# Optimization experiments

Measured on AMD Instinct MI355X. Metric: run time of the kernel, lower is better.

Reference implementation:

```python
import jax, jax.numpy as jnp
import numpy as np

K = 5  # kernel_size, n_qubits = K*K = 25
PAD = (K - 1) // 2  # 'same' padding, stride 1


def _extract_patches(x):
    """x: [B, C, H, W] -> [B, C, H, W, K*K] 5x5 patches, zero 'same' padding."""
    B, C, H, W = x.shape
    xp = jnp.pad(x, ((0, 0), (0, 0), (PAD, PAD), (PAD, PAD)))
    # 25 static shifted views stacked on a trailing axis (fixed small loop)
    return jnp.stack(
        [xp[:, :, di:di + H, dj:dj + W] for di in range(K) for dj in range(K)],
        axis=-1,
    )


def _vqc_1mout(patches, w):
    """Analytic expectation <Z_0> of the vqc_1mout circuit:
    AngleEmbedding (RX) of the 25 patch values, one BasicEntanglerLayer
    (per-wire RX(w_i) followed by a CNOT ring 0->1->...->24->0), measure Z on
    wire 0. Heisenberg-propagating Z_0 through the CNOT ring gives the tensor
    product of Z on wires 1..24 over the product state after the RX rotations,
    so <Z_0> = prod_{i=1..24} cos(x_i + w_i).
    patches: [..., 25], w: [25] -> out: [...].
    """
    y = jnp.cos(patches + w)  # broadcast over trailing 25
    return jnp.prod(y[..., 1:], axis=-1)


def setup_inputs() -> dict:
    key = jax.random.key(0)
    kx, kw = jax.random.split(key)
    x = jax.random.normal(kx, (32, 16, 64, 64), dtype=jnp.float32)
    # learned VQC rotation angles (n_qlayers=1, 25 qubits)
    w = jax.random.uniform(kw, (K * K,), dtype=jnp.float32,
                           minval=0.0, maxval=2.0 * np.pi)
    return {"x": x, "w": w}


def reference(x, w):
    # depthwise quanvolution: out[b, f, h, w] = VQC(5x5 patch of x[b, f])
    patches = _extract_patches(x)          # [B, C, H, W, 25]
    return _vqc_1mout(patches, w)          # [B, C, H, W]
```

## Files before the change

kernel.cpp:

```cpp
#include <hip/hip_runtime.h>
#include <hip/hip_bf16.h>
#include <math.h>


#define TR   32
#define SMR  (TR + 4)
#define SMC  (64 + 4)

__device__ __forceinline__ float rdlane(float v, int lane) {
    return __uint_as_float(__builtin_amdgcn_readlane(__float_as_uint(v), lane));
}

__global__ __launch_bounds__(256)
void qconv5x5_kernel(const float* __restrict__ x, const float* __restrict__ w,
                     float* __restrict__ out)
{
    __shared__ alignas(16) float2 sm[SMR][SMC];

    const int tid   = threadIdx.x;
    const int bid   = blockIdx.x;
    const int plane = bid >> 1;
    const int r0    = (bid & 1) * TR;

    const int lane = tid & 63;
    float sv, cv;
    __sincosf(w[lane < 25 ? lane : 0], &sv, &cv);
    float cw[25], sw[25];
#pragma unroll
    for (int p = 0; p < 25; ++p) {
        cw[p] = rdlane(cv, p);
        sw[p] = rdlane(sv, p);
    }

    const float* xp = x + plane * 64 * 64;
    for (int i = tid; i < SMR * SMC; i += 256) {
        const int rr = i / SMC;
        const int cc = i - rr * SMC;
        const int gr = r0 + rr - 2;
        const int gc = cc - 2;
        float c = 1.0f, s = 0.0f;
        if ((unsigned)gr < 64u && (unsigned)gc < 64u) {
            __sincosf(xp[gr * 64 + gc], &s, &c);
        }
        sm[rr][cc] = make_float2(c, s);
    }
    __syncthreads();

    const int cp = tid & 31;
    const int rq = tid >> 5;

    float prod[4][2];
#pragma unroll
    for (int ro = 0; ro < 4; ++ro) { prod[ro][0] = 1.f; prod[ro][1] = 1.f; }

#pragma unroll
    for (int nr = 0; nr < 8; ++nr) {
        const int tr = rq * 4 + nr;
        const float4* rowp = reinterpret_cast<const float4*>(&sm[tr][0]);
        float4 f0 = rowp[cp], f1 = rowp[cp + 1], f2 = rowp[cp + 2];
        float2 arr6[6] = { make_float2(f0.x, f0.y), make_float2(f0.z, f0.w),
                           make_float2(f1.x, f1.y), make_float2(f1.z, f1.w),
                           make_float2(f2.x, f2.y), make_float2(f2.z, f2.w) };
#pragma unroll
        for (int ro = 0; ro < 4; ++ro) {
            const int di = nr - ro;
            if (di < 0 || di > 4) continue;
#pragma unroll
            for (int dj = 0; dj < 5; ++dj) {
                const int p = di * 5 + dj;
#pragma unroll
                for (int pa = 0; pa < 2; ++pa) {
                    if (p == 0) continue;
                    const float2 v = arr6[dj + pa];
                    prod[ro][pa] *= fmaf(v.x, cw[p], -(v.y * sw[p]));
                }
            }
        }
    }

    float2* op = reinterpret_cast<float2*>(
        out + plane * 64 * 64 + (r0 + rq * 4) * 64 + 2 * cp);
#pragma unroll
    for (int ro = 0; ro < 4; ++ro)
        op[ro * 32] = make_float2(prod[ro][0], prod[ro][1]);
}

extern "C" void kernel_launch(void* const* d_in, const int* in_sizes, int n_in,
                              void* d_out, int out_size, void* d_ws, size_t ws_size,
                              hipStream_t stream) {
    const float* x = (const float*)d_in[0];
    const float* w = (const float*)d_in[1];
    float* out = (float*)d_out;
    (void)in_sizes; (void)n_in; (void)out_size; (void)d_ws; (void)ws_size;

    dim3 grid(512 * (64 / TR));
    dim3 block(256);
    qconv5x5_kernel<<<grid, block, 0, stream>>>(x, w, out);
}
```

Baseline: 65.69 us.

## Process whole plane per block with split cos/sin planes and packed-float math

```diff
diff --git a/kernel.cpp b/kernel.cpp
--- a/kernel.cpp
+++ b/kernel.cpp
@@ -3,9 +3,10 @@
 #include <math.h>
 
 
-#define TR   32
-#define SMR  (TR + 4)
-#define SMC  (64 + 4)
+#define SMR   68
+#define SMSTR 72
+
+typedef float v2f __attribute__((ext_vector_type(2)));
 
 __device__ __forceinline__ float rdlane(float v, int lane) {
     return __uint_as_float(__builtin_amdgcn_readlane(__float_as_uint(v), lane));
@@ -15,12 +16,11 @@
 void qconv5x5_kernel(const float* __restrict__ x, const float* __restrict__ w,
                      float* __restrict__ out)
 {
-    __shared__ alignas(16) float2 sm[SMR][SMC];
+    __shared__ alignas(16) float smc[SMR][SMSTR];
+    __shared__ alignas(16) float sms[SMR][SMSTR];
 
     const int tid   = threadIdx.x;
-    const int bid   = blockIdx.x;
-    const int plane = bid >> 1;
-    const int r0    = (bid & 1) * TR;
+    const int plane = blockIdx.x;
 
     const int lane = tid & 63;
     float sv, cv;
@@ -33,34 +33,36 @@
     }
 
     const float* xp = x + plane * 64 * 64;
-    for (int i = tid; i < SMR * SMC; i += 256) {
-        const int rr = i / SMC;
-        const int cc = i - rr * SMC;
-        const int gr = r0 + rr - 2;
+    for (int i = tid; i < SMR * SMR; i += 256) {
+        const int rr = i / SMR;
+        const int cc = i - rr * SMR;
+        const int gr = rr - 2;
         const int gc = cc - 2;
         float c = 1.0f, s = 0.0f;
         if ((unsigned)gr < 64u && (unsigned)gc < 64u) {
             __sincosf(xp[gr * 64 + gc], &s, &c);
         }
-        sm[rr][cc] = make_float2(c, s);
+        smc[rr][cc] = c;
+        sms[rr][cc] = s;
     }
     __syncthreads();
 
-    const int cp = tid & 31;
-    const int rq = tid >> 5;
+    const int ci = tid & 15;
+    const int rq = tid >> 4;
 
-    float prod[4][2];
+    v2f prodA[4], prodB[4];
 #pragma unroll
-    for (int ro = 0; ro < 4; ++ro) { prod[ro][0] = 1.f; prod[ro][1] = 1.f; }
+    for (int ro = 0; ro < 4; ++ro) { prodA[ro] = (v2f)1.0f; prodB[ro] = (v2f)1.0f; }
 
 #pragma unroll
     for (int nr = 0; nr < 8; ++nr) {
         const int tr = rq * 4 + nr;
-        const float4* rowp = reinterpret_cast<const float4*>(&sm[tr][0]);
-        float4 f0 = rowp[cp], f1 = rowp[cp + 1], f2 = rowp[cp + 2];
-        float2 arr6[6] = { make_float2(f0.x, f0.y), make_float2(f0.z, f0.w),
-                           make_float2(f1.x, f1.y), make_float2(f1.z, f1.w),
-                           make_float2(f2.x, f2.y), make_float2(f2.z, f2.w) };
+        const float4 c0 = *reinterpret_cast<const float4*>(&smc[tr][4 * ci]);
+        const float4 c1 = *reinterpret_cast<const float4*>(&smc[tr][4 * ci + 4]);
+        const float4 s0 = *reinterpret_cast<const float4*>(&sms[tr][4 * ci]);
+        const float4 s1 = *reinterpret_cast<const float4*>(&sms[tr][4 * ci + 4]);
+        const float cwin[8] = {c0.x, c0.y, c0.z, c0.w, c1.x, c1.y, c1.z, c1.w};
+        const float swin[8] = {s0.x, s0.y, s0.z, s0.w, s1.x, s1.y, s1.z, s1.w};
 #pragma unroll
         for (int ro = 0; ro < 4; ++ro) {
             const int di = nr - ro;
@@ -68,21 +70,23 @@
 #pragma unroll
             for (int dj = 0; dj < 5; ++dj) {
                 const int p = di * 5 + dj;
-#pragma unroll
-                for (int pa = 0; pa < 2; ++pa) {
-                    if (p == 0) continue;
-                    const float2 v = arr6[dj + pa];
-                    prod[ro][pa] *= fmaf(v.x, cw[p], -(v.y * sw[p]));
-                }
+                if (p == 0) continue;
+                v2f ca; ca.x = cwin[dj];     ca.y = cwin[dj + 1];
+                v2f cb; cb.x = cwin[dj + 2]; cb.y = cwin[dj + 3];
+                v2f sa; sa.x = swin[dj];     sa.y = swin[dj + 1];
+                v2f sb; sb.x = swin[dj + 2]; sb.y = swin[dj + 3];
+                prodA[ro] *= (ca * cw[p] - sa * sw[p]);
+                prodB[ro] *= (cb * cw[p] - sb * sw[p]);
             }
         }
     }
 
-    float2* op = reinterpret_cast<float2*>(
-        out + plane * 64 * 64 + (r0 + rq * 4) * 64 + 2 * cp);
+    float* op = out + plane * 64 * 64 + (rq * 4) * 64 + 4 * ci;
 #pragma unroll
-    for (int ro = 0; ro < 4; ++ro)
-        op[ro * 32] = make_float2(prod[ro][0], prod[ro][1]);
+    for (int ro = 0; ro < 4; ++ro) {
+        float4 v = make_float4(prodA[ro].x, prodA[ro].y, prodB[ro].x, prodB[ro].y);
+        *reinterpret_cast<float4*>(op + ro * 64) = v;
+    }
 }
 
 extern "C" void kernel_launch(void* const* d_in, const int* in_sizes, int n_in,
@@ -93,7 +97,7 @@
     float* out = (float*)d_out;
     (void)in_sizes; (void)n_in; (void)out_size; (void)d_ws; (void)ws_size;
 
-    dim3 grid(512 * (64 / TR));
+    dim3 grid(512);
     dim3 block(256);
     qconv5x5_kernel<<<grid, block, 0, stream>>>(x, w, out);
 }
```

New measurement: 68.46 us. 1.04x slower.

## Give each wave its own 16x32 tile with vectorized loads and wave barrier

Applied to the files above, without the earlier changes.

```diff
diff --git a/kernel.cpp b/kernel.cpp
--- a/kernel.cpp
+++ b/kernel.cpp
@@ -3,9 +3,8 @@
 #include <math.h>
 
 
-#define TR   32
-#define SMR  (TR + 4)
-#define SMC  (64 + 4)
+#define WROWS 20
+#define WCOLS 36
 
 __device__ __forceinline__ float rdlane(float v, int lane) {
     return __uint_as_float(__builtin_amdgcn_readlane(__float_as_uint(v), lane));
@@ -15,14 +14,18 @@
 void qconv5x5_kernel(const float* __restrict__ x, const float* __restrict__ w,
                      float* __restrict__ out)
 {
-    __shared__ alignas(16) float2 sm[SMR][SMC];
+    __shared__ alignas(16) float2 sm[4][WROWS][WCOLS];
 
-    const int tid   = threadIdx.x;
-    const int bid   = blockIdx.x;
-    const int plane = bid >> 1;
-    const int r0    = (bid & 1) * TR;
+    const int tid  = threadIdx.x;
+    const int lane = tid & 63;
+    const int q    = tid >> 6;
+    const int W    = blockIdx.x * 4 + q;
+    const int plane = W >> 3;
+    const int sub   = W & 7;
+    const int r0    = (sub >> 1) * 16;
+    const int h     = sub & 1;
+    const int c0    = h * 32;
 
-    const int lane = tid & 63;
     float sv, cv;
     __sincosf(w[lane < 25 ? lane : 0], &sv, &cv);
     float cw[25], sw[25];
@@ -33,21 +36,48 @@
     }
 
     const float* xp = x + plane * 64 * 64;
-    for (int i = tid; i < SMR * SMC; i += 256) {
-        const int rr = i / SMC;
-        const int cc = i - rr * SMC;
+    float2 (*R)[WCOLS] = sm[q];
+
+    for (int i = lane; i < WROWS * 10; i += 64) {
+        const int rr = i / 10;
+        const int t  = i - rr * 10;
         const int gr = r0 + rr - 2;
-        const int gc = cc - 2;
-        float c = 1.0f, s = 0.0f;
-        if ((unsigned)gr < 64u && (unsigned)gc < 64u) {
-            __sincosf(xp[gr * 64 + gc], &s, &c);
+        const bool rowok = (unsigned)gr < 64u;
+        const float* rowg = xp + gr * 64;
+        if (t < 8) {
+            float4 px = make_float4(0.f, 0.f, 0.f, 0.f);
+            if (rowok) px = *reinterpret_cast<const float4*>(rowg + c0 + 4 * t);
+            float s0, c0_, s1, c1_, s2, c2_, s3, c3_;
+            __sincosf(px.x, &s0, &c0_);
+            __sincosf(px.y, &s1, &c1_);
+            __sincosf(px.z, &s2, &c2_);
+            __sincosf(px.w, &s3, &c3_);
+            float2* dst = &R[rr][4 * t + 2];
+            *reinterpret_cast<float4*>(dst)     = make_float4(c0_, s0, c1_, s1);
+            *reinterpret_cast<float4*>(dst + 2) = make_float4(c2_, s2, c3_, s3);
+        } else if (t == 8) {
+            float2 px = make_float2(0.f, 0.f);
+            if (rowok && h == 1)
+                px = *reinterpret_cast<const float2*>(rowg + c0 - 2);
+            float sa, ca, sb, cb;
+            __sincosf((rowok && h == 1) ? px.x : 0.f, &sa, &ca);
+            __sincosf((rowok && h == 1) ? px.y : 0.f, &sb, &cb);
+            *reinterpret_cast<float4*>(&R[rr][0]) = make_float4(ca, sa, cb, sb);
+        } else {
+            float2 px = make_float2(0.f, 0.f);
+            if (rowok && h == 0)
+                px = *reinterpret_cast<const float2*>(rowg + c0 + 32);
+            float sa, ca, sb, cb;
+            __sincosf((rowok && h == 0) ? px.x : 0.f, &sa, &ca);
+            __sincosf((rowok && h == 0) ? px.y : 0.f, &sb, &cb);
+            *reinterpret_cast<float4*>(&R[rr][34]) = make_float4(ca, sa, cb, sb);
         }
-        sm[rr][cc] = make_float2(c, s);
     }
-    __syncthreads();
 
-    const int cp = tid & 31;
-    const int rq = tid >> 5;
+    __builtin_amdgcn_wave_barrier();
+
+    const int cp = lane & 15;
+    const int rg = lane >> 4;
 
     float prod[4][2];
 #pragma unroll
@@ -55,8 +85,8 @@
 
 #pragma unroll
     for (int nr = 0; nr < 8; ++nr) {
-        const int tr = rq * 4 + nr;
-        const float4* rowp = reinterpret_cast<const float4*>(&sm[tr][0]);
+        const int tr = rg * 4 + nr;
+        const float4* rowp = reinterpret_cast<const float4*>(&R[tr][0]);
         float4 f0 = rowp[cp], f1 = rowp[cp + 1], f2 = rowp[cp + 2];
         float2 arr6[6] = { make_float2(f0.x, f0.y), make_float2(f0.z, f0.w),
                            make_float2(f1.x, f1.y), make_float2(f1.z, f1.w),
@@ -79,7 +109,7 @@
     }
 
     float2* op = reinterpret_cast<float2*>(
-        out + plane * 64 * 64 + (r0 + rq * 4) * 64 + 2 * cp);
+        out + plane * 64 * 64 + (r0 + rg * 4) * 64 + c0 + 2 * cp);
 #pragma unroll
     for (int ro = 0; ro < 4; ++ro)
         op[ro * 32] = make_float2(prod[ro][0], prod[ro][1]);
@@ -93,7 +123,7 @@
     float* out = (float*)d_out;
     (void)in_sizes; (void)n_in; (void)out_size; (void)d_ws; (void)ws_size;
 
-    dim3 grid(512 * (64 / TR));
+    dim3 grid(1024);
     dim3 block(256);
     qconv5x5_kernel<<<grid, block, 0, stream>>>(x, w, out);
 }
```

Result: no change. 66.40 us (+1.1%).
